# Kernel optimization log

Measured on AMD Instinct MI355X. Metric: run time of the kernel, lower is better.

The kernel has to match this reference:

```python
import jax, jax.numpy as jnp
import numpy as np
from jax import lax

D_MODEL, D_STATE, D_CONV, EXPAND = 1024, 16, 4, 2
D_INNER = EXPAND * D_MODEL
B_SZ, L_SEQ = 2, 2048

# BitLinear quantization (BitNet b1.58 style, STE via stop_gradient)

def _weight_quant(w):
    scale = jnp.maximum(jnp.mean(jnp.abs(w)), 1e-5)
    q = jnp.clip(jnp.round(w / scale), -1.0, 1.0) * scale
    return w + lax.stop_gradient(q - w)

def _act_quant(x):
    s = 127.0 / jnp.maximum(jnp.max(jnp.abs(x), axis=-1, keepdims=True), 1e-5)
    q = jnp.clip(jnp.round(x * s), -128.0, 127.0) / s
    return x + lax.stop_gradient(q - x)

def bitlinear(x, w, b=None):
    y = _act_quant(x) @ _weight_quant(w).T
    return y + b if b is not None else y


def setup_inputs() -> dict:
    key = jax.random.key(0)
    ks = jax.random.split(key, 9)
    inp = {
        "x": jax.random.normal(ks[0], (B_SZ, L_SEQ, D_MODEL), jnp.float32),
        "in_proj_w": jax.random.normal(ks[1], (2 * D_INNER, D_MODEL), jnp.float32) * 0.02,
        "conv_w": jax.random.normal(ks[2], (D_INNER, 1, D_CONV), jnp.float32) * 0.2,
        "conv_b": jnp.zeros((D_INNER,), jnp.float32),
        "delta_w": jax.random.normal(ks[3], (D_STATE, D_INNER), jnp.float32) * 0.02,
        "delta_b": jnp.zeros((D_STATE,), jnp.float32),
        "B_w": jax.random.normal(ks[4], (D_STATE, D_INNER), jnp.float32) * 0.02,
        "C_w": jax.random.normal(ks[5], (D_STATE, D_INNER), jnp.float32) * 0.02,
        "out_w": jax.random.normal(ks[6], (D_MODEL, D_INNER), jnp.float32) * 0.02,
        "D": jnp.ones((D_INNER,), jnp.float32),
        "log_A": -0.5 * jnp.log(1.0 + jnp.arange(1, D_STATE + 1, dtype=jnp.float32) / D_STATE),
    }
    return inp


def reference(x, in_proj_w, conv_w, conv_b, delta_w, delta_b, B_w, C_w, out_w, D, log_A):
    B, L, _ = x.shape
    # input projection + SiLU gating
    xp = bitlinear(x, in_proj_w)                      # [B, L, 2*d_inner]
    x_gate, x_input = jnp.split(xp, 2, axis=-1)
    x_input = jax.nn.silu(x_gate) * x_input          # [B, L, d_inner]
    # causal depthwise conv1d (padding d_conv-1 then truncation == left-pad)
    xc = lax.conv_general_dilated(
        x_input.transpose(0, 2, 1), conv_w, window_strides=(1,),
        padding=[(D_CONV - 1, 0)], feature_group_count=D_INNER)
    x_input = (xc + conv_b[None, :, None]).transpose(0, 2, 1)  # [B, L, d_inner]
    # selective parameters
    delta = bitlinear(x_input, delta_w, delta_b)     # [B, L, N]
    A_d = jnp.exp(delta * log_A[None, None, :])      # [B, L, N]
    B_mat = bitlinear(x_input, B_w)                  # [B, L, N]
    C_mat = bitlinear(x_input, C_w)                  # [B, L, N]
    # diagonal state recurrence via lax.scan over time
    dB = delta * B_mat                               # [B, L, N]
    def step(h, ins):
        a_t, db_t, c_t = ins                         # each [B, N]
        h = a_t * h + db_t
        return h, jnp.sum(c_t * h, axis=-1)          # signal: [B]
    h0 = jnp.zeros((B, D_STATE), x.dtype)
    _, sig = lax.scan(step, h0, (A_d.transpose(1, 0, 2), dB.transpose(1, 0, 2), C_mat.transpose(1, 0, 2)))
    state_signal = sig.T[:, :, None]                 # [B, L, 1]
    y_inner = x_input * (jax.nn.sigmoid(state_signal) + D[None, None, :])
    return bitlinear(y_inner, out_w)                 # [B, L, d_model]
```

## Files before the change

kernel.cpp:

```cpp
#include <hip/hip_runtime.h>
#include <hip/hip_bf16.h>

typedef signed char i8;
typedef int v4i __attribute__((ext_vector_type(4)));

#define LSTR 80

__device__ __forceinline__ void gld16(const void* g, void* l) {
  __builtin_amdgcn_global_load_lds(
      (const __attribute__((address_space(1))) unsigned int*)g,
      (__attribute__((address_space(3))) unsigned int*)l, 16, 0, 0);
}

__global__ __launch_bounds__(256) void k_abssum_all(const float* __restrict__ w0, const float* __restrict__ w1,
                                                    const float* __restrict__ w2, const float* __restrict__ w3,
                                                    const float* __restrict__ w4, double* __restrict__ partial) {
  int b = blockIdx.x;
  const float* w; int n, nb, bg;
  if (b < 256)      { w = w0; n = 4194304; nb = 256; bg = b; }
  else if (b < 272) { w = w1; n = 32768;   nb = 16;  bg = b - 256; }
  else if (b < 288) { w = w2; n = 32768;   nb = 16;  bg = b - 272; }
  else if (b < 304) { w = w3; n = 32768;   nb = 16;  bg = b - 288; }
  else              { w = w4; n = 2097152; nb = 128; bg = b - 304; }
  __shared__ double sd[256];
  double acc = 0.0;
  for (int i = bg * 256 + threadIdx.x; i < n; i += nb * 256) acc += (double)fabsf(w[i]);
  sd[threadIdx.x] = acc;
  __syncthreads();
  for (int s = 128; s > 0; s >>= 1) {
    if (threadIdx.x < s) sd[threadIdx.x] += sd[threadIdx.x + s];
    __syncthreads();
  }
  if (threadIdx.x == 0) partial[b] = sd[0];
}

__global__ void k_finalize(const double* __restrict__ partial, float* __restrict__ scales) {
  int m = threadIdx.x;
  if (m >= 5) return;
  const int off[6] = {0, 256, 272, 288, 304, 432};
  const double cnt[5] = {4194304.0, 32768.0, 32768.0, 32768.0, 2097152.0};
  double s = 0.0;
  for (int i = off[m]; i < off[m + 1]; ++i) s += partial[i];
  scales[m] = fmaxf((float)(s / cnt[m]), 1e-5f);
}

__global__ __launch_bounds__(256) void k_wquant_all(const float* __restrict__ w0, const float* __restrict__ w1,
                                                    const float* __restrict__ w2, const float* __restrict__ w3,
                                                    const float* __restrict__ w4, const float* __restrict__ scales,
                                                    i8* __restrict__ tin, i8* __restrict__ t2, i8* __restrict__ tout) {
  int b = blockIdx.x;
  const float* w; i8* t; int m, n;
  if (b < 4096)      { w = w0; t = tin;          m = 0; n = 4194304; }
  else if (b < 4128) { w = w1; t = t2;           m = 1; n = 32768; b -= 4096; }
  else if (b < 4160) { w = w2; t = t2 + 32768;   m = 2; n = 32768; b -= 4128; }
  else if (b < 4192) { w = w3; t = t2 + 65536;   m = 3; n = 32768; b -= 4160; }
  else               { w = w4; t = tout;         m = 4; n = 2097152; b -= 4192; }
  int idx = (b * 256 + threadIdx.x) * 4;
  if (idx >= n) return;
  float scale = scales[m];
  float4 v = *(const float4*)(w + idx);
  char4 q;
  q.x = (i8)fminf(fmaxf(rintf(v.x / scale), -1.f), 1.f);
  q.y = (i8)fminf(fmaxf(rintf(v.y / scale), -1.f), 1.f);
  q.z = (i8)fminf(fmaxf(rintf(v.z / scale), -1.f), 1.f);
  q.w = (i8)fminf(fmaxf(rintf(v.w / scale), -1.f), 1.f);
  *(char4*)(t + idx) = q;
}

template <int W>
__global__ __launch_bounds__(256) void k_actquant(const float* __restrict__ x,
                                                  i8* __restrict__ q, float* __restrict__ srow) {
  constexpr int E = W / 256;
  const int r = blockIdx.x, tid = threadIdx.x;
  const float* xr = x + (size_t)r * W;
  float v[E];
  float m = 0.f;
#pragma unroll
  for (int j = 0; j < E; j += 4) {
    float4 t = *(const float4*)(xr + tid * E + j);
    v[j] = t.x; v[j + 1] = t.y; v[j + 2] = t.z; v[j + 3] = t.w;
    m = fmaxf(m, fmaxf(fmaxf(fabsf(t.x), fabsf(t.y)), fmaxf(fabsf(t.z), fabsf(t.w))));
  }
  __shared__ float sm[4];
  __shared__ float sbc;
#pragma unroll
  for (int off = 32; off > 0; off >>= 1) m = fmaxf(m, __shfl_xor(m, off));
  if ((tid & 63) == 0) sm[tid >> 6] = m;
  __syncthreads();
  if (tid == 0) {
    float mm = fmaxf(fmaxf(sm[0], sm[1]), fmaxf(sm[2], sm[3]));
    float s = 127.0f / fmaxf(mm, 1e-5f);
    sbc = s;
    srow[r] = s;
  }
  __syncthreads();
  float s = sbc;
#pragma unroll
  for (int j = 0; j < E; j += 4) {
    char4 c;
    c.x = (i8)fminf(fmaxf(rintf(v[j] * s), -128.f), 127.f);
    c.y = (i8)fminf(fmaxf(rintf(v[j + 1] * s), -128.f), 127.f);
    c.z = (i8)fminf(fmaxf(rintf(v[j + 2] * s), -128.f), 127.f);
    c.w = (i8)fminf(fmaxf(rintf(v[j + 3] * s), -128.f), 127.f);
    *(char4*)(q + (size_t)r * W + tid * E + j) = c;
  }
}

__global__ __launch_bounds__(256) void k_gemm1(const i8* __restrict__ qx, const i8* __restrict__ tin,
                                               const float* __restrict__ sx, const float* __restrict__ scales,
                                               float* __restrict__ gated) {
  __shared__ i8 As[16384], Bg[16384], Bv[16384];
  __shared__ float frow[128];
  const int tid = threadIdx.x;
  const int r0 = blockIdx.x * 128, c0 = blockIdx.y * 128;
  if (tid < 128) frow[tid] = scales[0] / sx[r0 + tid];
  const int lane = tid & 63, wv = tid >> 6;
  const int wr = wv >> 1, wc = wv & 1;
  const int lo = lane & 15, hi = lane >> 4;
  const int sr = tid >> 3;
  const int sp = tid & 7;
  v4i accg[4][4], accv[4][4];
#pragma unroll
  for (int m = 0; m < 4; ++m)
#pragma unroll
    for (int n = 0; n < 4; ++n) {
      accg[m][n] = (v4i){0, 0, 0, 0};
      accv[m][n] = (v4i){0, 0, 0, 0};
    }
  for (int kt = 0; kt < 8; ++kt) {
    const int kb = kt * 128;
    __syncthreads();
#pragma unroll
    for (int i = 0; i < 4; ++i) {
      int r = i * 32 + sr;
      int src = kb + ((sp ^ (r & 7)) << 4);
      int lds = i * 4096 + wv * 1024;
      gld16(qx + (size_t)(r0 + r) * 1024 + src, As + lds);
      gld16(tin + (size_t)(c0 + r) * 1024 + src, Bg + lds);
      gld16(tin + (size_t)(2048 + c0 + r) * 1024 + src, Bv + lds);
    }
    __syncthreads();
#pragma unroll
    for (int kh = 0; kh < 2; ++kh) {
      v4i a[4];
#pragma unroll
      for (int m = 0; m < 4; ++m) {
        int rr = wr * 64 + m * 16 + lo;
        int c = kh * 4 + hi;
        a[m] = *(const v4i*)&As[rr * 128 + ((c ^ (rr & 7)) << 4)];
      }
#pragma unroll
      for (int n = 0; n < 4; ++n) {
        int cc = wc * 64 + n * 16 + lo;
        int c = kh * 4 + hi;
        int off = cc * 128 + ((c ^ (cc & 7)) << 4);
        v4i bg = *(const v4i*)&Bg[off];
        v4i bv = *(const v4i*)&Bv[off];
#pragma unroll
        for (int m = 0; m < 4; ++m) {
          accg[m][n] = __builtin_amdgcn_mfma_i32_16x16x64_i8(a[m], bg, accg[m][n], 0, 0, 0);
          accv[m][n] = __builtin_amdgcn_mfma_i32_16x16x64_i8(a[m], bv, accv[m][n], 0, 0, 0);
        }
      }
    }
  }
#pragma unroll
  for (int m = 0; m < 4; ++m)
#pragma unroll
    for (int n = 0; n < 4; ++n)
#pragma unroll
      for (int rg = 0; rg < 4; ++rg) {
        int row = wr * 64 + m * 16 + hi * 4 + rg;
        int col = wc * 64 + n * 16 + lo;
        float f = frow[row];
        float g = (float)accg[m][n][rg] * f;
        float v = (float)accv[m][n][rg] * f;
        float sg = 1.0f / (1.0f + expf(-g));
        gated[(size_t)(r0 + row) * 2048 + c0 + col] = g * sg * v;
      }
}

__global__ __launch_bounds__(256) void k_convq(const float* __restrict__ g, const float* __restrict__ cw,
                                               const float* __restrict__ cb, float* __restrict__ xo,
                                               i8* __restrict__ q, float* __restrict__ srow) {
  const int tid = threadIdx.x;
  const int r0 = blockIdx.x * 8;
  const int l0 = r0 & 2047;
  const int ch = tid * 8;
  const int lane = tid & 63, wv = tid >> 6;
  float wt[4][8];
#pragma unroll
  for (int j = 0; j < 8; ++j) {
    float4 w = *(const float4*)(cw + (ch + j) * 4);
    wt[0][j] = w.x; wt[1][j] = w.y; wt[2][j] = w.z; wt[3][j] = w.w;
  }
  float bias[8];
  {
    float4 b0 = *(const float4*)(cb + ch), b1 = *(const float4*)(cb + ch + 4);
    bias[0] = b0.x; bias[1] = b0.y; bias[2] = b0.z; bias[3] = b0.w;
    bias[4] = b1.x; bias[5] = b1.y; bias[6] = b1.z; bias[7] = b1.w;
  }
  const float* gb = g + (size_t)r0 * 2048 + ch;
  float wm3[8], wm2[8], wm1[8];
  if (l0 != 0) {
    float4 a, b;
    a = *(const float4*)(gb - 3 * 2048); b = *(const float4*)(gb - 3 * 2048 + 4);
    wm3[0]=a.x; wm3[1]=a.y; wm3[2]=a.z; wm3[3]=a.w; wm3[4]=b.x; wm3[5]=b.y; wm3[6]=b.z; wm3[7]=b.w;
    a = *(const float4*)(gb - 2 * 2048); b = *(const float4*)(gb - 2 * 2048 + 4);
    wm2[0]=a.x; wm2[1]=a.y; wm2[2]=a.z; wm2[3]=a.w; wm2[4]=b.x; wm2[5]=b.y; wm2[6]=b.z; wm2[7]=b.w;
    a = *(const float4*)(gb - 1 * 2048); b = *(const float4*)(gb - 1 * 2048 + 4);
    wm1[0]=a.x; wm1[1]=a.y; wm1[2]=a.z; wm1[3]=a.w; wm1[4]=b.x; wm1[5]=b.y; wm1[6]=b.z; wm1[7]=b.w;
  } else {
#pragma unroll
    for (int j = 0; j < 8; ++j) { wm3[j] = 0.f; wm2[j] = 0.f; wm1[j] = 0.f; }
  }
  float* xop = xo + (size_t)r0 * 2048 + ch;
  float rowmax[8];
#pragma unroll
  for (int l = 0; l < 8; ++l) {
    float cur[8];
    {
      float4 a = *(const float4*)(gb + l * 2048), b = *(const float4*)(gb + l * 2048 + 4);
      cur[0]=a.x; cur[1]=a.y; cur[2]=a.z; cur[3]=a.w; cur[4]=b.x; cur[5]=b.y; cur[6]=b.z; cur[7]=b.w;
    }
    float acc[8];
    float m = 0.f;
#pragma unroll
    for (int j = 0; j < 8; ++j) {
      float v = bias[j];
      v = fmaf(wt[0][j], wm3[j], v);
      v = fmaf(wt[1][j], wm2[j], v);
      v = fmaf(wt[2][j], wm1[j], v);
      v = fmaf(wt[3][j], cur[j], v);
      acc[j] = v;
      m = fmaxf(m, fabsf(v));
    }
    rowmax[l] = m;
    *(float4*)(xop + l * 2048) = make_float4(acc[0], acc[1], acc[2], acc[3]);
    *(float4*)(xop + l * 2048 + 4) = make_float4(acc[4], acc[5], acc[6], acc[7]);
#pragma unroll
    for (int j = 0; j < 8; ++j) { wm3[j] = wm2[j]; wm2[j] = wm1[j]; wm1[j] = cur[j]; }
  }
  __shared__ float sred[8][4];
  __shared__ float sscale[8];
#pragma unroll
  for (int l = 0; l < 8; ++l) {
    float m = rowmax[l];
#pragma unroll
    for (int off = 32; off > 0; off >>= 1) m = fmaxf(m, __shfl_xor(m, off));
    if (lane == 0) sred[l][wv] = m;
  }
  __syncthreads();
  if (tid < 8) {
    float mm = fmaxf(fmaxf(sred[tid][0], sred[tid][1]), fmaxf(sred[tid][2], sred[tid][3]));
    float s = 127.0f / fmaxf(mm, 1e-5f);
    sscale[tid] = s;
    srow[r0 + tid] = s;
  }
  __syncthreads();
  i8* qp = q + (size_t)r0 * 2048 + ch;
#pragma unroll
  for (int l = 0; l < 8; ++l) {
    float s = sscale[l];
    float4 a = *(const float4*)(xop + l * 2048);
    float4 b = *(const float4*)(xop + l * 2048 + 4);
    char4 c0q, c1q;
    c0q.x = (i8)fminf(fmaxf(rintf(a.x * s), -128.f), 127.f);
    c0q.y = (i8)fminf(fmaxf(rintf(a.y * s), -128.f), 127.f);
    c0q.z = (i8)fminf(fmaxf(rintf(a.z * s), -128.f), 127.f);
    c0q.w = (i8)fminf(fmaxf(rintf(a.w * s), -128.f), 127.f);
    c1q.x = (i8)fminf(fmaxf(rintf(b.x * s), -128.f), 127.f);
    c1q.y = (i8)fminf(fmaxf(rintf(b.y * s), -128.f), 127.f);
    c1q.z = (i8)fminf(fmaxf(rintf(b.z * s), -128.f), 127.f);
    c1q.w = (i8)fminf(fmaxf(rintf(b.w * s), -128.f), 127.f);
    *(char4*)(qp + l * 2048) = c0q;
    *(char4*)(qp + l * 2048 + 4) = c1q;
  }
}

__global__ __launch_bounds__(256) void k_gemm2(const i8* __restrict__ q2, const i8* __restrict__ t2,
                                               int* __restrict__ ipart) {
  __shared__ i8 As[64 * LSTR];
  __shared__ i8 Bs[48 * LSTR];
  const int tid = threadIdx.x;
  const int r0 = blockIdx.x * 64;
  const int kb = blockIdx.y * 1024;
  const int lrow = tid >> 2, lk = (tid & 3) * 16;
  const int lane = tid & 63, wv = tid >> 6;
  const int fr = lane & 15, fk = (lane >> 4) * 16;
  v4i acc[3];
#pragma unroll
  for (int s = 0; s < 3; ++s) acc[s] = (v4i){0, 0, 0, 0};
  for (int ks = 0; ks < 16; ++ks) {
    const int k0 = kb + ks * 64;
    __syncthreads();
    *(v4i*)&As[lrow * LSTR + lk] = *(const v4i*)&q2[(size_t)(r0 + lrow) * 2048 + k0 + lk];
    if (tid < 192)
      *(v4i*)&Bs[(tid >> 2) * LSTR + (tid & 3) * 16] = *(const v4i*)&t2[(size_t)(tid >> 2) * 2048 + k0 + (tid & 3) * 16];
    __syncthreads();
    v4i a = *(const v4i*)&As[(wv * 16 + fr) * LSTR + fk];
#pragma unroll
    for (int s = 0; s < 3; ++s) {
      v4i b = *(const v4i*)&Bs[(s * 16 + fr) * LSTR + fk];
      acc[s] = __builtin_amdgcn_mfma_i32_16x16x64_i8(a, b, acc[s], 0, 0, 0);
    }
  }
#pragma unroll
  for (int s = 0; s < 3; ++s)
#pragma unroll
    for (int rg = 0; rg < 4; ++rg) {
      int row = wv * 16 + (lane >> 4) * 4 + rg;
      int col = s * 16 + (lane & 15);
      ipart[(size_t)blockIdx.y * 196608 + (size_t)(r0 + row) * 48 + col] = acc[s][rg];
    }
}

__global__ __launch_bounds__(256) void k_xform(const int* __restrict__ ip, const float* __restrict__ s2,
                                               const float* __restrict__ scales, const float* __restrict__ dbias,
                                               const float* __restrict__ logA, float* __restrict__ At,
                                               float* __restrict__ dBt, float* __restrict__ Ct) {
  int idx = blockIdx.x * 256 + threadIdx.x;
  int r = idx >> 4, n = idx & 15;
  int b = r >> 11, l = r & 2047;
  float fr = 1.0f / s2[r];
  int base = r * 48;
  float dd = (float)(ip[base + n] + ip[196608 + base + n]) * (scales[1] * fr) + dbias[n];
  float Bv = (float)(ip[base + 16 + n] + ip[196608 + base + 16 + n]) * (scales[2] * fr);
  float Cv = (float)(ip[base + 32 + n] + ip[196608 + base + 32 + n]) * (scales[3] * fr);
  int o = ((b * 16 + n) << 11) | l;
  At[o] = expf(dd * logA[n]);
  dBt[o] = dd * Bv;
  Ct[o] = Cv;
}

__global__ __launch_bounds__(256) void k_scan(const float* __restrict__ At, const float* __restrict__ dBt,
                                              const float* __restrict__ Ct, float* __restrict__ ch) {
  const int i = threadIdx.x;
  const int base = blockIdx.x << 11;
  float a[8], db[8], c[8];
  {
    const float4* p = (const float4*)(At + base + i * 8);
    float4 t0 = p[0], t1 = p[1];
    a[0]=t0.x; a[1]=t0.y; a[2]=t0.z; a[3]=t0.w; a[4]=t1.x; a[5]=t1.y; a[6]=t1.z; a[7]=t1.w;
  }
  {
    const float4* p = (const float4*)(dBt + base + i * 8);
    float4 t0 = p[0], t1 = p[1];
    db[0]=t0.x; db[1]=t0.y; db[2]=t0.z; db[3]=t0.w; db[4]=t1.x; db[5]=t1.y; db[6]=t1.z; db[7]=t1.w;
  }
  {
    const float4* p = (const float4*)(Ct + base + i * 8);
    float4 t0 = p[0], t1 = p[1];
    c[0]=t0.x; c[1]=t0.y; c[2]=t0.z; c[3]=t0.w; c[4]=t1.x; c[5]=t1.y; c[6]=t1.z; c[7]=t1.w;
  }
  float Ac = 1.f, Bc = 0.f;
#pragma unroll
  for (int j = 0; j < 8; ++j) { Bc = a[j] * Bc + db[j]; Ac *= a[j]; }
  __shared__ float sA[256], sB[256];
  sA[i] = Ac; sB[i] = Bc;
  __syncthreads();
  for (int off = 1; off < 256; off <<= 1) {
    float pA = 1.f, pB = 0.f;
    if (i >= off) { pA = sA[i - off]; pB = sB[i - off]; }
    __syncthreads();
    Bc = Ac * pB + Bc;
    Ac = Ac * pA;
    sA[i] = Ac; sB[i] = Bc;
    __syncthreads();
  }
  float h = (i > 0) ? sB[i - 1] : 0.f;
  float o[8];
#pragma unroll
  for (int j = 0; j < 8; ++j) { h = a[j] * h + db[j]; o[j] = c[j] * h; }
  float4* po = (float4*)(ch + base + i * 8);
  po[0] = make_float4(o[0], o[1], o[2], o[3]);
  po[1] = make_float4(o[4], o[5], o[6], o[7]);
}

__global__ __launch_bounds__(256) void k_yq(const float* __restrict__ xin, const float* __restrict__ chb,
                                            const float* __restrict__ Dp, i8* __restrict__ q,
                                            float* __restrict__ srow) {
  const int tid = threadIdx.x;
  const int r0 = blockIdx.x * 8;
  const int b = r0 >> 11, l0 = r0 & 2047;
  const int lane = tid & 63, wv = tid >> 6;
  __shared__ float ssig[8 * 16];
  __shared__ float ssg[8];
  __shared__ float sred[8][4];
  __shared__ float sscale[8];
  if (tid < 128) {
    int n = tid >> 3, li = tid & 7;
    ssig[li * 16 + n] = chb[((size_t)(b * 16 + n) << 11) | (l0 + li)];
  }
  __syncthreads();
  if (tid < 8) {
    float s = 0.f;
    for (int n = 0; n < 16; ++n) s += ssig[tid * 16 + n];
    ssg[tid] = 1.0f / (1.0f + expf(-s));
  }
  __syncthreads();
  const int ch = tid * 8;
  float dreg[8];
  {
    float4 d0 = *(const float4*)(Dp + ch), d1 = *(const float4*)(Dp + ch + 4);
    dreg[0]=d0.x; dreg[1]=d0.y; dreg[2]=d0.z; dreg[3]=d0.w;
    dreg[4]=d1.x; dreg[5]=d1.y; dreg[6]=d1.z; dreg[7]=d1.w;
  }
  const float* xr = xin + (size_t)r0 * 2048 + ch;
  float rowmax[8];
#pragma unroll
  for (int l = 0; l < 8; ++l) {
    float sg = ssg[l];
    float4 a = *(const float4*)(xr + l * 2048);
    float4 c = *(const float4*)(xr + l * 2048 + 4);
    float m = 0.f;
    m = fmaxf(m, fabsf(a.x * (sg + dreg[0])));
    m = fmaxf(m, fabsf(a.y * (sg + dreg[1])));
    m = fmaxf(m, fabsf(a.z * (sg + dreg[2])));
    m = fmaxf(m, fabsf(a.w * (sg + dreg[3])));
    m = fmaxf(m, fabsf(c.x * (sg + dreg[4])));
    m = fmaxf(m, fabsf(c.y * (sg + dreg[5])));
    m = fmaxf(m, fabsf(c.z * (sg + dreg[6])));
    m = fmaxf(m, fabsf(c.w * (sg + dreg[7])));
    rowmax[l] = m;
  }
#pragma unroll
  for (int l = 0; l < 8; ++l) {
    float m = rowmax[l];
#pragma unroll
    for (int off = 32; off > 0; off >>= 1) m = fmaxf(m, __shfl_xor(m, off));
    if (lane == 0) sred[l][wv] = m;
  }
  __syncthreads();
  if (tid < 8) {
    float mm = fmaxf(fmaxf(sred[tid][0], sred[tid][1]), fmaxf(sred[tid][2], sred[tid][3]));
    float s = 127.0f / fmaxf(mm, 1e-5f);
    sscale[tid] = s;
    srow[r0 + tid] = s;
  }
  __syncthreads();
  i8* qp = q + (size_t)r0 * 2048 + ch;
#pragma unroll
  for (int l = 0; l < 8; ++l) {
    float s = sscale[l];
    float sg = ssg[l];
    float4 a = *(const float4*)(xr + l * 2048);
    float4 c = *(const float4*)(xr + l * 2048 + 4);
    char4 c0q, c1q;
    c0q.x = (i8)fminf(fmaxf(rintf(a.x * (sg + dreg[0]) * s), -128.f), 127.f);
    c0q.y = (i8)fminf(fmaxf(rintf(a.y * (sg + dreg[1]) * s), -128.f), 127.f);
    c0q.z = (i8)fminf(fmaxf(rintf(a.z * (sg + dreg[2]) * s), -128.f), 127.f);
    c0q.w = (i8)fminf(fmaxf(rintf(a.w * (sg + dreg[3]) * s), -128.f), 127.f);
    c1q.x = (i8)fminf(fmaxf(rintf(c.x * (sg + dreg[4]) * s), -128.f), 127.f);
    c1q.y = (i8)fminf(fmaxf(rintf(c.y * (sg + dreg[5]) * s), -128.f), 127.f);
    c1q.z = (i8)fminf(fmaxf(rintf(c.z * (sg + dreg[6]) * s), -128.f), 127.f);
    c1q.w = (i8)fminf(fmaxf(rintf(c.w * (sg + dreg[7]) * s), -128.f), 127.f);
    *(char4*)(qp + l * 2048) = c0q;
    *(char4*)(qp + l * 2048 + 4) = c1q;
  }
}

__global__ __launch_bounds__(256) void k_gemm3(const i8* __restrict__ q3, const i8* __restrict__ tout,
                                               const float* __restrict__ s3, const float* __restrict__ scales,
                                               float* __restrict__ out) {
  __shared__ i8 As[16384], Bs[16384];
  __shared__ float frow[128];
  const int tid = threadIdx.x;
  const int r0 = blockIdx.x * 128, c0 = blockIdx.y * 128;
  if (tid < 128) frow[tid] = scales[4] / s3[r0 + tid];
  const int lane = tid & 63, wv = tid >> 6;
  const int wr = wv >> 1, wc = wv & 1;
  const int lo = lane & 15, hi = lane >> 4;
  const int sr = tid >> 3;
  const int sp = tid & 7;
  v4i acc[4][4];
#pragma unroll
  for (int m = 0; m < 4; ++m)
#pragma unroll
    for (int n = 0; n < 4; ++n) acc[m][n] = (v4i){0, 0, 0, 0};
  for (int kt = 0; kt < 16; ++kt) {
    const int kb = kt * 128;
    __syncthreads();
#pragma unroll
    for (int i = 0; i < 4; ++i) {
      int r = i * 32 + sr;
      int src = kb + ((sp ^ (r & 7)) << 4);
      int lds = i * 4096 + wv * 1024;
      gld16(q3 + (size_t)(r0 + r) * 2048 + src, As + lds);
      gld16(tout + (size_t)(c0 + r) * 2048 + src, Bs + lds);
    }
    __syncthreads();
#pragma unroll
    for (int kh = 0; kh < 2; ++kh) {
      v4i a[4];
#pragma unroll
      for (int m = 0; m < 4; ++m) {
        int rr = wr * 64 + m * 16 + lo;
        int c = kh * 4 + hi;
        a[m] = *(const v4i*)&As[rr * 128 + ((c ^ (rr & 7)) << 4)];
      }
#pragma unroll
      for (int n = 0; n < 4; ++n) {
        int cc = wc * 64 + n * 16 + lo;
        int c = kh * 4 + hi;
        v4i b = *(const v4i*)&Bs[cc * 128 + ((c ^ (cc & 7)) << 4)];
#pragma unroll
        for (int m = 0; m < 4; ++m)
          acc[m][n] = __builtin_amdgcn_mfma_i32_16x16x64_i8(a[m], b, acc[m][n], 0, 0, 0);
      }
    }
  }
#pragma unroll
  for (int m = 0; m < 4; ++m)
#pragma unroll
    for (int n = 0; n < 4; ++n)
#pragma unroll
      for (int rg = 0; rg < 4; ++rg) {
        int row = wr * 64 + m * 16 + hi * 4 + rg;
        int col = wc * 64 + n * 16 + lo;
        out[(size_t)(r0 + row) * 1024 + c0 + col] = (float)acc[m][n][rg] * frow[row];
      }
}

extern "C" void kernel_launch(void* const* d_in, const int* in_sizes, int n_in,
                              void* d_out, int out_size, void* d_ws, size_t ws_size,
                              hipStream_t stream) {
  const float* x     = (const float*)d_in[0];
  const float* win   = (const float*)d_in[1];
  const float* cw    = (const float*)d_in[2];
  const float* cb    = (const float*)d_in[3];
  const float* dw    = (const float*)d_in[4];
  const float* dbias = (const float*)d_in[5];
  const float* bw    = (const float*)d_in[6];
  const float* cmw   = (const float*)d_in[7];
  const float* ow    = (const float*)d_in[8];
  const float* Dp    = (const float*)d_in[9];
  const float* logA  = (const float*)d_in[10];
  float* out = (float*)d_out;

  char* p = (char*)d_ws;
  float* gated = (float*)p;   p += (size_t)4096 * 2048 * 4;
  float* xin   = (float*)p;   p += (size_t)4096 * 2048 * 4;
  char* qx_rgn = p;           p += (size_t)4096 * 1024;
  char* tin_rgn = p;          p += (size_t)2 * 2048 * 1024;
  i8* tout = (i8*)p;          p += (size_t)1024 * 2048;
  i8* t2   = (i8*)p;          p += (size_t)48 * 2048;
  i8* q2   = (i8*)p;          p += (size_t)4096 * 2048;
  i8* q3   = (i8*)p;          p += (size_t)4096 * 2048;
  float* sx  = (float*)p;     p += (size_t)4096 * 4;
  float* s2  = (float*)p;     p += (size_t)4096 * 4;
  float* s3  = (float*)p;     p += (size_t)4096 * 4;
  float* scales = (float*)p;  p += 256;
  double* partial = (double*)p;

  i8* qx  = (i8*)qx_rgn;
  i8* tin = (i8*)tin_rgn;
  int* ipart = (int*)qx_rgn;
  float* At  = (float*)tin_rgn;
  float* dBt = At + 65536;
  float* Ct  = dBt + 65536;
  float* chb = Ct + 65536;

  k_abssum_all<<<432, 256, 0, stream>>>(win, dw, bw, cmw, ow, partial);
  k_finalize<<<1, 64, 0, stream>>>(partial, scales);
  k_wquant_all<<<6240, 256, 0, stream>>>(win, dw, bw, cmw, ow, scales, tin, t2, tout);

  k_actquant<1024><<<4096, 256, 0, stream>>>(x, qx, sx);
  k_gemm1<<<dim3(32, 16), 256, 0, stream>>>(qx, tin, sx, scales, gated);
  k_convq<<<512, 256, 0, stream>>>(gated, cw, cb, xin, q2, s2);
  k_gemm2<<<dim3(64, 2), 256, 0, stream>>>(q2, t2, ipart);
  k_xform<<<256, 256, 0, stream>>>(ipart, s2, scales, dbias, logA, At, dBt, Ct);
  k_scan<<<32, 256, 0, stream>>>(At, dBt, Ct, chb);
  k_yq<<<512, 256, 0, stream>>>(xin, chb, Dp, q3, s3);
  k_gemm3<<<dim3(32, 8), 256, 0, stream>>>(q3, tout, s3, scales, out);
}
```

Measured before the change: 163.6 us.

## Double-buffer LDS tiles in int8 GEMMs to overlap global loads with MFMA

```diff
diff --git a/kernel.cpp b/kernel.cpp
--- a/kernel.cpp
+++ b/kernel.cpp
@@ -106,19 +106,45 @@
   }
 }
 
+#define COMPUTE1(Ab, Gb, Vb)                                                        \
+  {                                                                                 \
+    v4i a[4];                                                                       \
+    _Pragma("unroll") for (int m = 0; m < 4; ++m) {                                 \
+      int rr = wr * 64 + m * 16 + lo;                                               \
+      a[m] = *(const v4i*)&Ab[rr * 64 + ((hi ^ (rr & 3)) << 4)];                    \
+    }                                                                               \
+    __builtin_amdgcn_s_setprio(1);                                                  \
+    _Pragma("unroll") for (int n = 0; n < 4; ++n) {                                 \
+      int cc = wc * 64 + n * 16 + lo;                                               \
+      int off = cc * 64 + ((hi ^ (cc & 3)) << 4);                                   \
+      v4i bg = *(const v4i*)&Gb[off];                                               \
+      v4i bv = *(const v4i*)&Vb[off];                                               \
+      _Pragma("unroll") for (int m = 0; m < 4; ++m) {                               \
+        accg[m][n] = __builtin_amdgcn_mfma_i32_16x16x64_i8(a[m], bg, accg[m][n], 0, 0, 0); \
+        accv[m][n] = __builtin_amdgcn_mfma_i32_16x16x64_i8(a[m], bv, accv[m][n], 0, 0, 0); \
+      }                                                                             \
+    }                                                                               \
+    __builtin_amdgcn_s_setprio(0);                                                  \
+  }
+
+#define SYNCPIPE                                             \
+  asm volatile("s_waitcnt vmcnt(0)" ::: "memory");           \
+  __builtin_amdgcn_s_barrier();
+
 __global__ __launch_bounds__(256) void k_gemm1(const i8* __restrict__ qx, const i8* __restrict__ tin,
                                                const float* __restrict__ sx, const float* __restrict__ scales,
                                                float* __restrict__ gated) {
-  __shared__ i8 As[16384], Bg[16384], Bv[16384];
+  __shared__ i8 A0[8192], A1[8192], G0[8192], G1[8192], V0[8192], V1[8192];
   __shared__ float frow[128];
   const int tid = threadIdx.x;
   const int r0 = blockIdx.x * 128, c0 = blockIdx.y * 128;
   if (tid < 128) frow[tid] = scales[0] / sx[r0 + tid];
+  __syncthreads();
   const int lane = tid & 63, wv = tid >> 6;
   const int wr = wv >> 1, wc = wv & 1;
   const int lo = lane & 15, hi = lane >> 4;
-  const int sr = tid >> 3;
-  const int sp = tid & 7;
+  const int srw = wv * 16 + (lane >> 2);
+  const int sc = lane & 3;
   v4i accg[4][4], accv[4][4];
 #pragma unroll
   for (int m = 0; m < 4; ++m)
@@ -127,43 +153,33 @@
       accg[m][n] = (v4i){0, 0, 0, 0};
       accv[m][n] = (v4i){0, 0, 0, 0};
     }
-  for (int kt = 0; kt < 8; ++kt) {
-    const int kb = kt * 128;
-    __syncthreads();
-#pragma unroll
-    for (int i = 0; i < 4; ++i) {
-      int r = i * 32 + sr;
-      int src = kb + ((sp ^ (r & 7)) << 4);
-      int lds = i * 4096 + wv * 1024;
-      gld16(qx + (size_t)(r0 + r) * 1024 + src, As + lds);
-      gld16(tin + (size_t)(c0 + r) * 1024 + src, Bg + lds);
-      gld16(tin + (size_t)(2048 + c0 + r) * 1024 + src, Bv + lds);
-    }
-    __syncthreads();
-#pragma unroll
-    for (int kh = 0; kh < 2; ++kh) {
-      v4i a[4];
-#pragma unroll
-      for (int m = 0; m < 4; ++m) {
-        int rr = wr * 64 + m * 16 + lo;
-        int c = kh * 4 + hi;
-        a[m] = *(const v4i*)&As[rr * 128 + ((c ^ (rr & 7)) << 4)];
-      }
-#pragma unroll
-      for (int n = 0; n < 4; ++n) {
-        int cc = wc * 64 + n * 16 + lo;
-        int c = kh * 4 + hi;
-        int off = cc * 128 + ((c ^ (cc & 7)) << 4);
-        v4i bg = *(const v4i*)&Bg[off];
-        v4i bv = *(const v4i*)&Bv[off];
-#pragma unroll
-        for (int m = 0; m < 4; ++m) {
-          accg[m][n] = __builtin_amdgcn_mfma_i32_16x16x64_i8(a[m], bg, accg[m][n], 0, 0, 0);
-          accv[m][n] = __builtin_amdgcn_mfma_i32_16x16x64_i8(a[m], bv, accv[m][n], 0, 0, 0);
-        }
-      }
-    }
-  }
+
+#define STAGE1(kt, Ab, Gb, Vb)                                           \
+  {                                                                      \
+    const int kb = (kt)*64;                                              \
+    _Pragma("unroll") for (int i = 0; i < 2; ++i) {                      \
+      int r = i * 64 + srw;                                              \
+      int src = kb + ((sc ^ (r & 3)) << 4);                              \
+      int db = i * 4096 + wv * 1024;                                     \
+      gld16(qx + (size_t)(r0 + r) * 1024 + src, Ab + db);                \
+      gld16(tin + (size_t)(c0 + r) * 1024 + src, Gb + db);               \
+      gld16(tin + (size_t)(2048 + c0 + r) * 1024 + src, Vb + db);        \
+    }                                                                    \
+  }
+
+  STAGE1(0, A0, G0, V0);
+  SYNCPIPE;
+#pragma unroll
+  for (int kt = 0; kt < 16; kt += 2) {
+    STAGE1(kt + 1, A1, G1, V1);
+    COMPUTE1(A0, G0, V0);
+    SYNCPIPE;
+    if (kt + 2 < 16) STAGE1(kt + 2, A0, G0, V0);
+    COMPUTE1(A1, G1, V1);
+    SYNCPIPE;
+  }
+#undef STAGE1
+
 #pragma unroll
   for (int m = 0; m < 4; ++m)
 #pragma unroll
@@ -460,56 +476,68 @@
   }
 }
 
+#define COMPUTE3(Ab, Bb)                                                            \
+  {                                                                                 \
+    v4i a[4];                                                                       \
+    _Pragma("unroll") for (int m = 0; m < 4; ++m) {                                 \
+      int rr = wr * 64 + m * 16 + lo;                                               \
+      a[m] = *(const v4i*)&Ab[rr * 64 + ((hi ^ (rr & 3)) << 4)];                    \
+    }                                                                               \
+    __builtin_amdgcn_s_setprio(1);                                                  \
+    _Pragma("unroll") for (int n = 0; n < 4; ++n) {                                 \
+      int cc = wc * 64 + n * 16 + lo;                                               \
+      v4i b = *(const v4i*)&Bb[cc * 64 + ((hi ^ (cc & 3)) << 4)];                   \
+      _Pragma("unroll") for (int m = 0; m < 4; ++m)                                 \
+        acc[m][n] = __builtin_amdgcn_mfma_i32_16x16x64_i8(a[m], b, acc[m][n], 0, 0, 0); \
+    }                                                                               \
+    __builtin_amdgcn_s_setprio(0);                                                  \
+  }
+
 __global__ __launch_bounds__(256) void k_gemm3(const i8* __restrict__ q3, const i8* __restrict__ tout,
                                                const float* __restrict__ s3, const float* __restrict__ scales,
                                                float* __restrict__ out) {
-  __shared__ i8 As[16384], Bs[16384];
+  __shared__ i8 A0[8192], A1[8192], B0[8192], B1[8192];
   __shared__ float frow[128];
   const int tid = threadIdx.x;
   const int r0 = blockIdx.x * 128, c0 = blockIdx.y * 128;
   if (tid < 128) frow[tid] = scales[4] / s3[r0 + tid];
+  __syncthreads();
   const int lane = tid & 63, wv = tid >> 6;
   const int wr = wv >> 1, wc = wv & 1;
   const int lo = lane & 15, hi = lane >> 4;
-  const int sr = tid >> 3;
-  const int sp = tid & 7;
+  const int srw = wv * 16 + (lane >> 2);
+  const int sc = lane & 3;
   v4i acc[4][4];
 #pragma unroll
   for (int m = 0; m < 4; ++m)
 #pragma unroll
     for (int n = 0; n < 4; ++n) acc[m][n] = (v4i){0, 0, 0, 0};
-  for (int kt = 0; kt < 16; ++kt) {
-    const int kb = kt * 128;
-    __syncthreads();
-#pragma unroll
-    for (int i = 0; i < 4; ++i) {
-      int r = i * 32 + sr;
-      int src = kb + ((sp ^ (r & 7)) << 4);
-      int lds = i * 4096 + wv * 1024;
-      gld16(q3 + (size_t)(r0 + r) * 2048 + src, As + lds);
-      gld16(tout + (size_t)(c0 + r) * 2048 + src, Bs + lds);
-    }
-    __syncthreads();
-#pragma unroll
-    for (int kh = 0; kh < 2; ++kh) {
-      v4i a[4];
-#pragma unroll
-      for (int m = 0; m < 4; ++m) {
-        int rr = wr * 64 + m * 16 + lo;
-        int c = kh * 4 + hi;
-        a[m] = *(const v4i*)&As[rr * 128 + ((c ^ (rr & 7)) << 4)];
-      }
-#pragma unroll
-      for (int n = 0; n < 4; ++n) {
-        int cc = wc * 64 + n * 16 + lo;
-        int c = kh * 4 + hi;
-        v4i b = *(const v4i*)&Bs[cc * 128 + ((c ^ (cc & 7)) << 4)];
-#pragma unroll
-        for (int m = 0; m < 4; ++m)
-          acc[m][n] = __builtin_amdgcn_mfma_i32_16x16x64_i8(a[m], b, acc[m][n], 0, 0, 0);
-      }
-    }
-  }
+
+#define STAGE3(kt, Ab, Bb)                                               \
+  {                                                                      \
+    const int kb = (kt)*64;                                              \
+    _Pragma("unroll") for (int i = 0; i < 2; ++i) {                      \
+      int r = i * 64 + srw;                                              \
+      int src = kb + ((sc ^ (r & 3)) << 4);                              \
+      int db = i * 4096 + wv * 1024;                                     \
+      gld16(q3 + (size_t)(r0 + r) * 2048 + src, Ab + db);                \
+      gld16(tout + (size_t)(c0 + r) * 2048 + src, Bb + db);              \
+    }                                                                    \
+  }
+
+  STAGE3(0, A0, B0);
+  SYNCPIPE;
+#pragma unroll
+  for (int kt = 0; kt < 32; kt += 2) {
+    STAGE3(kt + 1, A1, B1);
+    COMPUTE3(A0, B0);
+    SYNCPIPE;
+    if (kt + 2 < 32) STAGE3(kt + 2, A0, B0);
+    COMPUTE3(A1, B1);
+    SYNCPIPE;
+  }
+#undef STAGE3
+
 #pragma unroll
   for (int m = 0; m < 4; ++m)
 #pragma unroll
```

New measurement: 152.0 us. 1.08x faster.

## Triple-buffer int8 GEMM LDS tiles with async prefetch and halve gemm3 row tile

Applied to the files above, without the earlier changes.

```diff
diff --git a/kernel.cpp b/kernel.cpp
--- a/kernel.cpp
+++ b/kernel.cpp
@@ -11,6 +11,8 @@
       (const __attribute__((address_space(1))) unsigned int*)g,
       (__attribute__((address_space(3))) unsigned int*)l, 16, 0, 0);
 }
+
+#define LADDR(rr, c) ((((rr) >> 1) << 7) + (((rr) & 1) << 6) + ((((c) ^ (((rr) >> 1) & 3))) << 4))
 
 __global__ __launch_bounds__(256) void k_abssum_all(const float* __restrict__ w0, const float* __restrict__ w1,
                                                     const float* __restrict__ w2, const float* __restrict__ w3,
@@ -109,7 +111,7 @@
 __global__ __launch_bounds__(256) void k_gemm1(const i8* __restrict__ qx, const i8* __restrict__ tin,
                                                const float* __restrict__ sx, const float* __restrict__ scales,
                                                float* __restrict__ gated) {
-  __shared__ i8 As[16384], Bg[16384], Bv[16384];
+  __shared__ i8 A_[3][8192], G_[3][8192], V_[3][8192];
   __shared__ float frow[128];
   const int tid = threadIdx.x;
   const int r0 = blockIdx.x * 128, c0 = blockIdx.y * 128;
@@ -117,8 +119,8 @@
   const int lane = tid & 63, wv = tid >> 6;
   const int wr = wv >> 1, wc = wv & 1;
   const int lo = lane & 15, hi = lane >> 4;
-  const int sr = tid >> 3;
-  const int sp = tid & 7;
+  const int sr_ = wv * 16 + (lane >> 2);
+  const int scs = ((lane & 3) ^ ((lane >> 3) & 3)) << 4;
   v4i accg[4][4], accv[4][4];
 #pragma unroll
   for (int m = 0; m < 4; ++m)
@@ -127,43 +129,56 @@
       accg[m][n] = (v4i){0, 0, 0, 0};
       accv[m][n] = (v4i){0, 0, 0, 0};
     }
-  for (int kt = 0; kt < 8; ++kt) {
-    const int kb = kt * 128;
-    __syncthreads();
-#pragma unroll
-    for (int i = 0; i < 4; ++i) {
-      int r = i * 32 + sr;
-      int src = kb + ((sp ^ (r & 7)) << 4);
-      int lds = i * 4096 + wv * 1024;
-      gld16(qx + (size_t)(r0 + r) * 1024 + src, As + lds);
-      gld16(tin + (size_t)(c0 + r) * 1024 + src, Bg + lds);
-      gld16(tin + (size_t)(2048 + c0 + r) * 1024 + src, Bv + lds);
+
+#define STAGE1(kt, bi)                                                      \
+  {                                                                         \
+    const int kb = (kt)*64;                                                 \
+    _Pragma("unroll") for (int i = 0; i < 2; ++i) {                         \
+      int r = i * 64 + sr_;                                                 \
+      int dst = i * 4096 + wv * 1024;                                       \
+      gld16(qx + (size_t)(r0 + r) * 1024 + kb + scs, A_[bi] + dst);         \
+      gld16(tin + (size_t)(c0 + r) * 1024 + kb + scs, G_[bi] + dst);        \
+      gld16(tin + (size_t)(2048 + c0 + r) * 1024 + kb + scs, V_[bi] + dst); \
+    }                                                                       \
+  }
+
+#define COMPUTE1(bi)                                                                         \
+  {                                                                                          \
+    v4i a[4];                                                                                \
+    _Pragma("unroll") for (int m = 0; m < 4; ++m) {                                          \
+      int rr = wr * 64 + m * 16 + lo;                                                        \
+      a[m] = *(const v4i*)&A_[bi][LADDR(rr, hi)];                                            \
+    }                                                                                        \
+    __builtin_amdgcn_s_setprio(1);                                                           \
+    _Pragma("unroll") for (int n = 0; n < 4; ++n) {                                          \
+      int cc = wc * 64 + n * 16 + lo;                                                        \
+      int off = LADDR(cc, hi);                                                               \
+      v4i bg = *(const v4i*)&G_[bi][off];                                                    \
+      v4i bv = *(const v4i*)&V_[bi][off];                                                    \
+      _Pragma("unroll") for (int m = 0; m < 4; ++m) {                                        \
+        accg[m][n] = __builtin_amdgcn_mfma_i32_16x16x64_i8(a[m], bg, accg[m][n], 0, 0, 0);   \
+        accv[m][n] = __builtin_amdgcn_mfma_i32_16x16x64_i8(a[m], bv, accv[m][n], 0, 0, 0);   \
+      }                                                                                      \
+    }                                                                                        \
+    __builtin_amdgcn_s_setprio(0);                                                           \
+  }
+
+  STAGE1(0, 0);
+  STAGE1(1, 1);
+#pragma unroll
+  for (int kt = 0; kt < 16; ++kt) {
+    if (kt < 15) {
+      asm volatile("s_waitcnt vmcnt(6)" ::: "memory");
+    } else {
+      asm volatile("s_waitcnt vmcnt(0)" ::: "memory");
     }
-    __syncthreads();
-#pragma unroll
-    for (int kh = 0; kh < 2; ++kh) {
-      v4i a[4];
-#pragma unroll
-      for (int m = 0; m < 4; ++m) {
-        int rr = wr * 64 + m * 16 + lo;
-        int c = kh * 4 + hi;
-        a[m] = *(const v4i*)&As[rr * 128 + ((c ^ (rr & 7)) << 4)];
-      }
-#pragma unroll
-      for (int n = 0; n < 4; ++n) {
-        int cc = wc * 64 + n * 16 + lo;
-        int c = kh * 4 + hi;
-        int off = cc * 128 + ((c ^ (cc & 7)) << 4);
-        v4i bg = *(const v4i*)&Bg[off];
-        v4i bv = *(const v4i*)&Bv[off];
-#pragma unroll
-        for (int m = 0; m < 4; ++m) {
-          accg[m][n] = __builtin_amdgcn_mfma_i32_16x16x64_i8(a[m], bg, accg[m][n], 0, 0, 0);
-          accv[m][n] = __builtin_amdgcn_mfma_i32_16x16x64_i8(a[m], bv, accv[m][n], 0, 0, 0);
-        }
-      }
-    }
-  }
+    __builtin_amdgcn_s_barrier();
+    if (kt + 2 < 16) STAGE1(kt + 2, (kt + 2) % 3);
+    COMPUTE1(kt % 3);
+  }
+#undef STAGE1
+#undef COMPUTE1
+
 #pragma unroll
   for (int m = 0; m < 4; ++m)
 #pragma unroll
@@ -463,60 +478,73 @@
 __global__ __launch_bounds__(256) void k_gemm3(const i8* __restrict__ q3, const i8* __restrict__ tout,
                                                const float* __restrict__ s3, const float* __restrict__ scales,
                                                float* __restrict__ out) {
-  __shared__ i8 As[16384], Bs[16384];
-  __shared__ float frow[128];
+  __shared__ i8 A_[3][4096], B_[3][8192];
+  __shared__ float frow[64];
   const int tid = threadIdx.x;
-  const int r0 = blockIdx.x * 128, c0 = blockIdx.y * 128;
-  if (tid < 128) frow[tid] = scales[4] / s3[r0 + tid];
+  const int r0 = blockIdx.x * 64, c0 = blockIdx.y * 128;
+  if (tid < 64) frow[tid] = scales[4] / s3[r0 + tid];
   const int lane = tid & 63, wv = tid >> 6;
   const int wr = wv >> 1, wc = wv & 1;
   const int lo = lane & 15, hi = lane >> 4;
-  const int sr = tid >> 3;
-  const int sp = tid & 7;
-  v4i acc[4][4];
-#pragma unroll
-  for (int m = 0; m < 4; ++m)
+  const int sr_ = wv * 16 + (lane >> 2);
+  const int scs = ((lane & 3) ^ ((lane >> 3) & 3)) << 4;
+  v4i acc[2][4];
+#pragma unroll
+  for (int m = 0; m < 2; ++m)
 #pragma unroll
     for (int n = 0; n < 4; ++n) acc[m][n] = (v4i){0, 0, 0, 0};
-  for (int kt = 0; kt < 16; ++kt) {
-    const int kb = kt * 128;
-    __syncthreads();
-#pragma unroll
-    for (int i = 0; i < 4; ++i) {
-      int r = i * 32 + sr;
-      int src = kb + ((sp ^ (r & 7)) << 4);
-      int lds = i * 4096 + wv * 1024;
-      gld16(q3 + (size_t)(r0 + r) * 2048 + src, As + lds);
-      gld16(tout + (size_t)(c0 + r) * 2048 + src, Bs + lds);
+
+#define STAGE3(kt, bi)                                                       \
+  {                                                                          \
+    const int kb = (kt)*64;                                                  \
+    gld16(q3 + (size_t)(r0 + sr_) * 2048 + kb + scs, A_[bi] + wv * 1024);    \
+    _Pragma("unroll") for (int i = 0; i < 2; ++i) {                          \
+      int r = i * 64 + sr_;                                                  \
+      gld16(tout + (size_t)(c0 + r) * 2048 + kb + scs,                       \
+            B_[bi] + i * 4096 + wv * 1024);                                  \
+    }                                                                        \
+  }
+
+#define COMPUTE3(bi)                                                                       \
+  {                                                                                        \
+    v4i a[2];                                                                              \
+    _Pragma("unroll") for (int m = 0; m < 2; ++m) {                                        \
+      int rr = wr * 32 + m * 16 + lo;                                                      \
+      a[m] = *(const v4i*)&A_[bi][LADDR(rr, hi)];                                          \
+    }                                                                                      \
+    __builtin_amdgcn_s_setprio(1);                                                         \
+    _Pragma("unroll") for (int n = 0; n < 4; ++n) {                                        \
+      int cc = wc * 64 + n * 16 + lo;                                                      \
+      v4i b = *(const v4i*)&B_[bi][LADDR(cc, hi)];                                         \
+      _Pragma("unroll") for (int m = 0; m < 2; ++m)                                        \
+        acc[m][n] = __builtin_amdgcn_mfma_i32_16x16x64_i8(a[m], b, acc[m][n], 0, 0, 0);    \
+    }                                                                                      \
+    __builtin_amdgcn_s_setprio(0);                                                         \
+  }
+
+  STAGE3(0, 0);
+  STAGE3(1, 1);
+#pragma unroll
+  for (int kt = 0; kt < 32; ++kt) {
+    if (kt < 31) {
+      asm volatile("s_waitcnt vmcnt(3)" ::: "memory");
+    } else {
+      asm volatile("s_waitcnt vmcnt(0)" ::: "memory");
     }
-    __syncthreads();
-#pragma unroll
-    for (int kh = 0; kh < 2; ++kh) {
-      v4i a[4];
-#pragma unroll
-      for (int m = 0; m < 4; ++m) {
-        int rr = wr * 64 + m * 16 + lo;
-        int c = kh * 4 + hi;
-        a[m] = *(const v4i*)&As[rr * 128 + ((c ^ (rr & 7)) << 4)];
-      }
-#pragma unroll
-      for (int n = 0; n < 4; ++n) {
-        int cc = wc * 64 + n * 16 + lo;
-        int c = kh * 4 + hi;
-        v4i b = *(const v4i*)&Bs[cc * 128 + ((c ^ (cc & 7)) << 4)];
-#pragma unroll
-        for (int m = 0; m < 4; ++m)
-          acc[m][n] = __builtin_amdgcn_mfma_i32_16x16x64_i8(a[m], b, acc[m][n], 0, 0, 0);
-      }
-    }
-  }
-#pragma unroll
-  for (int m = 0; m < 4; ++m)
+    __builtin_amdgcn_s_barrier();
+    if (kt + 2 < 32) STAGE3(kt + 2, (kt + 2) % 3);
+    COMPUTE3(kt % 3);
+  }
+#undef STAGE3
+#undef COMPUTE3
+
+#pragma unroll
+  for (int m = 0; m < 2; ++m)
 #pragma unroll
     for (int n = 0; n < 4; ++n)
 #pragma unroll
       for (int rg = 0; rg < 4; ++rg) {
-        int row = wr * 64 + m * 16 + hi * 4 + rg;
+        int row = wr * 32 + m * 16 + hi * 4 + rg;
         int col = wc * 64 + n * 16 + lo;
         out[(size_t)(r0 + row) * 1024 + c0 + col] = (float)acc[m][n][rg] * frow[row];
       }
@@ -572,5 +600,5 @@
   k_xform<<<256, 256, 0, stream>>>(ipart, s2, scales, dbias, logA, At, dBt, Ct);
   k_scan<<<32, 256, 0, stream>>>(At, dBt, Ct, chb);
   k_yq<<<512, 256, 0, stream>>>(xin, chb, Dp, q3, s3);
-  k_gemm3<<<dim3(32, 8), 256, 0, stream>>>(q3, tout, s3, scales, out);
-}
+  k_gemm3<<<dim3(64, 8), 256, 0, stream>>>(q3, tout, s3, scales, out);
+}
```

New measurement: 162.6 us. About the same (-0.6%).

## Double-buffer int8 GEMM1/GEMM3 with 8-wave blocks and barrier-interleaved MFMA phases

Applied to the files above, without the earlier changes.

```diff
diff --git a/kernel.cpp b/kernel.cpp
--- a/kernel.cpp
+++ b/kernel.cpp
@@ -11,6 +11,10 @@
       (const __attribute__((address_space(1))) unsigned int*)g,
       (__attribute__((address_space(3))) unsigned int*)l, 16, 0, 0);
 }
+
+#define LADDR(rr, c) ((((rr) >> 1) << 7) + (((rr) & 1) << 6) + ((((c) ^ (((rr) >> 1) & 3))) << 4))
+
+#define MFMA_I8 __builtin_amdgcn_mfma_i32_16x16x64_i8
 
 __global__ __launch_bounds__(256) void k_abssum_all(const float* __restrict__ w0, const float* __restrict__ w1,
                                                     const float* __restrict__ w2, const float* __restrict__ w3,
@@ -106,19 +110,25 @@
   }
 }
 
-__global__ __launch_bounds__(256) void k_gemm1(const i8* __restrict__ qx, const i8* __restrict__ tin,
+__global__ __launch_bounds__(512) void k_gemm1(const i8* __restrict__ qx, const i8* __restrict__ tin,
                                                const float* __restrict__ sx, const float* __restrict__ scales,
                                                float* __restrict__ gated) {
-  __shared__ i8 As[16384], Bg[16384], Bv[16384];
-  __shared__ float frow[128];
+  __shared__ i8 A_[2][16384], G_[2][8192], V_[2][8192];
+  __shared__ float frow[256];
   const int tid = threadIdx.x;
-  const int r0 = blockIdx.x * 128, c0 = blockIdx.y * 128;
-  if (tid < 128) frow[tid] = scales[0] / sx[r0 + tid];
+  const int r0 = blockIdx.x * 256, c0 = blockIdx.y * 128;
+  if (tid < 256) frow[tid] = scales[0] / sx[r0 + tid];
   const int lane = tid & 63, wv = tid >> 6;
-  const int wr = wv >> 1, wc = wv & 1;
+  const int wm = wv >> 1, wn = wv & 1;
   const int lo = lane & 15, hi = lane >> 4;
-  const int sr = tid >> 3;
-  const int sp = tid & 7;
+  const int d0 = tid << 4;
+  const int sr0 = ((d0 >> 7) << 1) | ((d0 >> 6) & 1);
+  const int sc0 = ((((d0 >> 4) & 3) ^ ((sr0 >> 1) & 3)) << 4);
+  const i8* gA0 = qx + (size_t)(r0 + sr0) * 1024 + sc0;
+  const i8* gA1 = qx + (size_t)(r0 + 128 + sr0) * 1024 + sc0;
+  const i8* gG  = tin + (size_t)(c0 + sr0) * 1024 + sc0;
+  const i8* gV  = tin + (size_t)(2048 + c0 + sr0) * 1024 + sc0;
+  const int ldsb = wv << 10;
   v4i accg[4][4], accv[4][4];
 #pragma unroll
   for (int m = 0; m < 4; ++m)
@@ -127,51 +137,84 @@
       accg[m][n] = (v4i){0, 0, 0, 0};
       accv[m][n] = (v4i){0, 0, 0, 0};
     }
-  for (int kt = 0; kt < 8; ++kt) {
-    const int kb = kt * 128;
-    __syncthreads();
-#pragma unroll
-    for (int i = 0; i < 4; ++i) {
-      int r = i * 32 + sr;
-      int src = kb + ((sp ^ (r & 7)) << 4);
-      int lds = i * 4096 + wv * 1024;
-      gld16(qx + (size_t)(r0 + r) * 1024 + src, As + lds);
-      gld16(tin + (size_t)(c0 + r) * 1024 + src, Bg + lds);
-      gld16(tin + (size_t)(2048 + c0 + r) * 1024 + src, Bv + lds);
-    }
-    __syncthreads();
-#pragma unroll
-    for (int kh = 0; kh < 2; ++kh) {
-      v4i a[4];
-#pragma unroll
-      for (int m = 0; m < 4; ++m) {
-        int rr = wr * 64 + m * 16 + lo;
-        int c = kh * 4 + hi;
-        a[m] = *(const v4i*)&As[rr * 128 + ((c ^ (rr & 7)) << 4)];
-      }
-#pragma unroll
-      for (int n = 0; n < 4; ++n) {
-        int cc = wc * 64 + n * 16 + lo;
-        int c = kh * 4 + hi;
-        int off = cc * 128 + ((c ^ (cc & 7)) << 4);
-        v4i bg = *(const v4i*)&Bg[off];
-        v4i bv = *(const v4i*)&Bv[off];
-#pragma unroll
-        for (int m = 0; m < 4; ++m) {
-          accg[m][n] = __builtin_amdgcn_mfma_i32_16x16x64_i8(a[m], bg, accg[m][n], 0, 0, 0);
-          accv[m][n] = __builtin_amdgcn_mfma_i32_16x16x64_i8(a[m], bv, accv[m][n], 0, 0, 0);
-        }
-      }
-    }
-  }
+
+#define STAGE1(t, bi)                              \
+  {                                                \
+    const int kb = (t) << 6;                       \
+    gld16(gA0 + kb, A_[bi] + ldsb);                \
+    gld16(gA1 + kb, A_[bi] + 8192 + ldsb);         \
+    gld16(gG + kb, G_[bi] + ldsb);                 \
+    gld16(gV + kb, V_[bi] + ldsb);                 \
+  }
+
+  STAGE1(0, 0);
+  for (int t = 0; t < 16; ++t) {
+    const int bi = t & 1;
+    if (t < 15) {
+      STAGE1(t + 1, bi ^ 1);
+      asm volatile("s_waitcnt vmcnt(4)" ::: "memory");
+    } else {
+      asm volatile("s_waitcnt vmcnt(0)" ::: "memory");
+    }
+    __builtin_amdgcn_s_barrier();
+    v4i a[4];
+#pragma unroll
+    for (int m = 0; m < 4; ++m) a[m] = *(const v4i*)&A_[bi][LADDR(wm * 64 + m * 16 + lo, hi)];
+    v4i b0 = *(const v4i*)&G_[bi][LADDR(wn * 64 + lo, hi)];
+    v4i b1 = *(const v4i*)&G_[bi][LADDR(wn * 64 + 16 + lo, hi)];
+    __builtin_amdgcn_s_barrier();
+    __builtin_amdgcn_s_setprio(1);
+#pragma unroll
+    for (int m = 0; m < 4; ++m) {
+      accg[m][0] = MFMA_I8(a[m], b0, accg[m][0], 0, 0, 0);
+      accg[m][1] = MFMA_I8(a[m], b1, accg[m][1], 0, 0, 0);
+    }
+    __builtin_amdgcn_s_setprio(0);
+    __builtin_amdgcn_s_barrier();
+    b0 = *(const v4i*)&G_[bi][LADDR(wn * 64 + 32 + lo, hi)];
+    b1 = *(const v4i*)&G_[bi][LADDR(wn * 64 + 48 + lo, hi)];
+    __builtin_amdgcn_s_barrier();
+    __builtin_amdgcn_s_setprio(1);
+#pragma unroll
+    for (int m = 0; m < 4; ++m) {
+      accg[m][2] = MFMA_I8(a[m], b0, accg[m][2], 0, 0, 0);
+      accg[m][3] = MFMA_I8(a[m], b1, accg[m][3], 0, 0, 0);
+    }
+    __builtin_amdgcn_s_setprio(0);
+    __builtin_amdgcn_s_barrier();
+    b0 = *(const v4i*)&V_[bi][LADDR(wn * 64 + lo, hi)];
+    b1 = *(const v4i*)&V_[bi][LADDR(wn * 64 + 16 + lo, hi)];
+    __builtin_amdgcn_s_barrier();
+    __builtin_amdgcn_s_setprio(1);
+#pragma unroll
+    for (int m = 0; m < 4; ++m) {
+      accv[m][0] = MFMA_I8(a[m], b0, accv[m][0], 0, 0, 0);
+      accv[m][1] = MFMA_I8(a[m], b1, accv[m][1], 0, 0, 0);
+    }
+    __builtin_amdgcn_s_setprio(0);
+    __builtin_amdgcn_s_barrier();
+    b0 = *(const v4i*)&V_[bi][LADDR(wn * 64 + 32 + lo, hi)];
+    b1 = *(const v4i*)&V_[bi][LADDR(wn * 64 + 48 + lo, hi)];
+    __builtin_amdgcn_s_barrier();
+    __builtin_amdgcn_s_setprio(1);
+#pragma unroll
+    for (int m = 0; m < 4; ++m) {
+      accv[m][2] = MFMA_I8(a[m], b0, accv[m][2], 0, 0, 0);
+      accv[m][3] = MFMA_I8(a[m], b1, accv[m][3], 0, 0, 0);
+    }
+    __builtin_amdgcn_s_setprio(0);
+    __builtin_amdgcn_s_barrier();
+  }
+#undef STAGE1
+
 #pragma unroll
   for (int m = 0; m < 4; ++m)
 #pragma unroll
     for (int n = 0; n < 4; ++n)
 #pragma unroll
       for (int rg = 0; rg < 4; ++rg) {
-        int row = wr * 64 + m * 16 + hi * 4 + rg;
-        int col = wc * 64 + n * 16 + lo;
+        int row = wm * 64 + m * 16 + hi * 4 + rg;
+        int col = wn * 64 + n * 16 + lo;
         float f = frow[row];
         float g = (float)accg[m][n][rg] * f;
         float v = (float)accv[m][n][rg] * f;
@@ -302,7 +345,7 @@
 #pragma unroll
     for (int s = 0; s < 3; ++s) {
       v4i b = *(const v4i*)&Bs[(s * 16 + fr) * LSTR + fk];
-      acc[s] = __builtin_amdgcn_mfma_i32_16x16x64_i8(a, b, acc[s], 0, 0, 0);
+      acc[s] = MFMA_I8(a, b, acc[s], 0, 0, 0);
     }
   }
 #pragma unroll
@@ -460,64 +503,82 @@
   }
 }
 
-__global__ __launch_bounds__(256) void k_gemm3(const i8* __restrict__ q3, const i8* __restrict__ tout,
+__global__ __launch_bounds__(512) void k_gemm3(const i8* __restrict__ q3, const i8* __restrict__ tout,
                                                const float* __restrict__ s3, const float* __restrict__ scales,
                                                float* __restrict__ out) {
-  __shared__ i8 As[16384], Bs[16384];
+  __shared__ i8 A_[2][8192], B_[2][8192];
   __shared__ float frow[128];
   const int tid = threadIdx.x;
   const int r0 = blockIdx.x * 128, c0 = blockIdx.y * 128;
   if (tid < 128) frow[tid] = scales[4] / s3[r0 + tid];
   const int lane = tid & 63, wv = tid >> 6;
-  const int wr = wv >> 1, wc = wv & 1;
+  const int wm = wv >> 1, wn = wv & 1;
   const int lo = lane & 15, hi = lane >> 4;
-  const int sr = tid >> 3;
-  const int sp = tid & 7;
-  v4i acc[4][4];
-#pragma unroll
-  for (int m = 0; m < 4; ++m)
+  const int d0 = tid << 4;
+  const int sr0 = ((d0 >> 7) << 1) | ((d0 >> 6) & 1);
+  const int sc0 = ((((d0 >> 4) & 3) ^ ((sr0 >> 1) & 3)) << 4);
+  const i8* gA = q3 + (size_t)(r0 + sr0) * 2048 + sc0;
+  const i8* gB = tout + (size_t)(c0 + sr0) * 2048 + sc0;
+  const int ldsb = wv << 10;
+  v4i acc[2][4];
+#pragma unroll
+  for (int m = 0; m < 2; ++m)
 #pragma unroll
     for (int n = 0; n < 4; ++n) acc[m][n] = (v4i){0, 0, 0, 0};
-  for (int kt = 0; kt < 16; ++kt) {
-    const int kb = kt * 128;
-    __syncthreads();
-#pragma unroll
-    for (int i = 0; i < 4; ++i) {
-      int r = i * 32 + sr;
-      int src = kb + ((sp ^ (r & 7)) << 4);
-      int lds = i * 4096 + wv * 1024;
-      gld16(q3 + (size_t)(r0 + r) * 2048 + src, As + lds);
-      gld16(tout + (size_t)(c0 + r) * 2048 + src, Bs + lds);
-    }
-    __syncthreads();
-#pragma unroll
-    for (int kh = 0; kh < 2; ++kh) {
-      v4i a[4];
-#pragma unroll
-      for (int m = 0; m < 4; ++m) {
-        int rr = wr * 64 + m * 16 + lo;
-        int c = kh * 4 + hi;
-        a[m] = *(const v4i*)&As[rr * 128 + ((c ^ (rr & 7)) << 4)];
-      }
-#pragma unroll
-      for (int n = 0; n < 4; ++n) {
-        int cc = wc * 64 + n * 16 + lo;
-        int c = kh * 4 + hi;
-        v4i b = *(const v4i*)&Bs[cc * 128 + ((c ^ (cc & 7)) << 4)];
-#pragma unroll
-        for (int m = 0; m < 4; ++m)
-          acc[m][n] = __builtin_amdgcn_mfma_i32_16x16x64_i8(a[m], b, acc[m][n], 0, 0, 0);
-      }
-    }
-  }
-#pragma unroll
-  for (int m = 0; m < 4; ++m)
+
+#define STAGE3(t, bi)                       \
+  {                                         \
+    const int kb = (t) << 6;                \
+    gld16(gA + kb, A_[bi] + ldsb);          \
+    gld16(gB + kb, B_[bi] + ldsb);          \
+  }
+
+  STAGE3(0, 0);
+  for (int t = 0; t < 32; ++t) {
+    const int bi = t & 1;
+    if (t < 31) {
+      STAGE3(t + 1, bi ^ 1);
+      asm volatile("s_waitcnt vmcnt(2)" ::: "memory");
+    } else {
+      asm volatile("s_waitcnt vmcnt(0)" ::: "memory");
+    }
+    __builtin_amdgcn_s_barrier();
+    v4i a[2];
+#pragma unroll
+    for (int m = 0; m < 2; ++m) a[m] = *(const v4i*)&A_[bi][LADDR(wm * 32 + m * 16 + lo, hi)];
+    v4i b0 = *(const v4i*)&B_[bi][LADDR(wn * 64 + lo, hi)];
+    v4i b1 = *(const v4i*)&B_[bi][LADDR(wn * 64 + 16 + lo, hi)];
+    __builtin_amdgcn_s_barrier();
+    __builtin_amdgcn_s_setprio(1);
+#pragma unroll
+    for (int m = 0; m < 2; ++m) {
+      acc[m][0] = MFMA_I8(a[m], b0, acc[m][0], 0, 0, 0);
+      acc[m][1] = MFMA_I8(a[m], b1, acc[m][1], 0, 0, 0);
+    }
+    __builtin_amdgcn_s_setprio(0);
+    __builtin_amdgcn_s_barrier();
+    b0 = *(const v4i*)&B_[bi][LADDR(wn * 64 + 32 + lo, hi)];
+    b1 = *(const v4i*)&B_[bi][LADDR(wn * 64 + 48 + lo, hi)];
+    __builtin_amdgcn_s_barrier();
+    __builtin_amdgcn_s_setprio(1);
+#pragma unroll
+    for (int m = 0; m < 2; ++m) {
+      acc[m][2] = MFMA_I8(a[m], b0, acc[m][2], 0, 0, 0);
+      acc[m][3] = MFMA_I8(a[m], b1, acc[m][3], 0, 0, 0);
+    }
+    __builtin_amdgcn_s_setprio(0);
+    __builtin_amdgcn_s_barrier();
+  }
+#undef STAGE3
+
+#pragma unroll
+  for (int m = 0; m < 2; ++m)
 #pragma unroll
     for (int n = 0; n < 4; ++n)
 #pragma unroll
       for (int rg = 0; rg < 4; ++rg) {
-        int row = wr * 64 + m * 16 + hi * 4 + rg;
-        int col = wc * 64 + n * 16 + lo;
+        int row = wm * 32 + m * 16 + hi * 4 + rg;
+        int col = wn * 64 + n * 16 + lo;
         out[(size_t)(r0 + row) * 1024 + c0 + col] = (float)acc[m][n][rg] * frow[row];
       }
 }
@@ -566,11 +627,11 @@
   k_wquant_all<<<6240, 256, 0, stream>>>(win, dw, bw, cmw, ow, scales, tin, t2, tout);
 
   k_actquant<1024><<<4096, 256, 0, stream>>>(x, qx, sx);
-  k_gemm1<<<dim3(32, 16), 256, 0, stream>>>(qx, tin, sx, scales, gated);
+  k_gemm1<<<dim3(16, 16), 512, 0, stream>>>(qx, tin, sx, scales, gated);
   k_convq<<<512, 256, 0, stream>>>(gated, cw, cb, xin, q2, s2);
   k_gemm2<<<dim3(64, 2), 256, 0, stream>>>(q2, t2, ipart);
   k_xform<<<256, 256, 0, stream>>>(ipart, s2, scales, dbias, logA, At, dBt, Ct);
   k_scan<<<32, 256, 0, stream>>>(At, dBt, Ct, chb);
   k_yq<<<512, 256, 0, stream>>>(xin, chb, Dp, q3, s3);
-  k_gemm3<<<dim3(32, 8), 256, 0, stream>>>(q3, tout, s3, scales, out);
-}
+  k_gemm3<<<dim3(32, 8), 512, 0, stream>>>(q3, tout, s3, scales, out);
+}
```

Measured after the change: 157.3 us. 3.8% less time.
